# Kernel tuning notes

Hardware: AMD Instinct MI355X
Metric: run time of the kernel (lower is better)

The kernel has to match this reference:

```python
import jax, jax.numpy as jnp
import numpy as np
from jax import lax

B, Ltok, DIM = 8, 4096, 384
D_STATE, D_CONV, EXPAND = 64, 4, 2
D_IN = EXPAND * DIM              # 768
DT_RANK = (DIM + 15) // 16       # 24
HID = 4 * DIM                    # 1536


def setup_inputs() -> dict:
    key = jax.random.key(0)
    ks = jax.random.split(key, 16)
    std = 0.02
    inp = {
        "x": jax.random.normal(ks[0], (B, Ltok, DIM), jnp.float32),
        "h": 64,
        "w": 64,
        # MambaLayer: pre-norm
        "gamma1": jnp.ones((DIM,), jnp.float32),
        "beta1": jnp.zeros((DIM,), jnp.float32),
        # Mamba params
        "W_in": jax.random.normal(ks[1], (2 * D_IN, DIM), jnp.float32) * std,
        "conv_w": jax.random.normal(ks[2], (D_IN, D_CONV), jnp.float32) * (1.0 / np.sqrt(D_CONV)),
        "conv_b": jnp.zeros((D_IN,), jnp.float32),
        "W_xproj": jax.random.normal(ks[3], (DT_RANK + 2 * D_STATE, D_IN), jnp.float32) * std,
        "W_dt": jax.random.normal(ks[4], (D_IN, DT_RANK), jnp.float32) * (DT_RANK ** -0.5),
        "b_dt": jax.random.uniform(ks[5], (D_IN,), jnp.float32, -4.0, -2.0),  # softplus -> small dt
        "A_log": jnp.tile(jnp.log(jnp.arange(1, D_STATE + 1, dtype=jnp.float32)), (D_IN, 1)),
        "Dp": jnp.ones((D_IN,), jnp.float32),
        "W_out": jax.random.normal(ks[6], (DIM, D_IN), jnp.float32) * std,
        # FFN branch
        "gamma2": jnp.ones((DIM,), jnp.float32),
        "beta2": jnp.zeros((DIM,), jnp.float32),
        "W1": jax.random.normal(ks[7], (HID, DIM), jnp.float32) * std,
        "b1": jnp.zeros((HID,), jnp.float32),
        "dw_w": jax.random.normal(ks[8], (HID, 3, 3), jnp.float32) * np.sqrt(2.0 / 9.0),
        "dw_b": jnp.zeros((HID,), jnp.float32),
        "W2": jax.random.normal(ks[9], (DIM, HID), jnp.float32) * std,
        "b2": jnp.zeros((DIM,), jnp.float32),
    }
    return inp


def _layer_norm(x, g, b, eps=1e-5):
    mu = x.mean(-1, keepdims=True)
    var = ((x - mu) ** 2).mean(-1, keepdims=True)
    return (x - mu) * lax.rsqrt(var + eps) * g + b


def _mamba(xn, W_in, conv_w, conv_b, W_xproj, W_dt, b_dt, A_log, Dp, W_out):
    b = xn.shape[0]
    xz = xn @ W_in.T                      # (b, l, 2*d_in)
    xr, z = jnp.split(xz, 2, axis=-1)
    # causal depthwise conv over seq
    xc = jnp.transpose(xr, (0, 2, 1))     # (b, d_in, l)
    xc = lax.conv_general_dilated(xc, conv_w[:, None, :], (1,), [(D_CONV - 1, 0)],
                                  feature_group_count=D_IN) + conv_b[None, :, None]
    xc = jax.nn.silu(jnp.transpose(xc, (0, 2, 1)))  # (b, l, d_in)
    xdb = xc @ W_xproj.T                  # (b, l, dt_rank + 2*d_state)
    dt = jax.nn.softplus(xdb[..., :DT_RANK] @ W_dt.T + b_dt)          # (b, l, d_in)
    Bm = xdb[..., DT_RANK:DT_RANK + D_STATE]                          # (b, l, d_state)
    Cm = xdb[..., DT_RANK + D_STATE:]                                 # (b, l, d_state)
    A = -jnp.exp(A_log)                   # (d_in, d_state)

    def step(hst, inp):
        dt_t, B_t, C_t, x_t = inp         # (b,d_in),(b,ds),(b,ds),(b,d_in)
        dA = jnp.exp(dt_t[..., None] * A)                 # (b, d_in, d_state)
        hst = hst * dA + (dt_t * x_t)[..., None] * B_t[:, None, :]
        y = jnp.einsum('bds,bs->bd', hst, C_t)
        return hst, y

    h0 = jnp.zeros((b, D_IN, D_STATE), xn.dtype)
    seq = (jnp.moveaxis(dt, 1, 0), jnp.moveaxis(Bm, 1, 0),
           jnp.moveaxis(Cm, 1, 0), jnp.moveaxis(xc, 1, 0))
    _, ys = lax.scan(step, h0, seq)
    y = jnp.moveaxis(ys, 0, 1) + xc * Dp  # (b, l, d_in)
    y = y * jax.nn.silu(z)
    return y @ W_out.T


def reference(x, h, w, gamma1, beta1, W_in, conv_w, conv_b, W_xproj, W_dt, b_dt,
              A_log, Dp, W_out, gamma2, beta2, W1, b1, dw_w, dw_b, W2, b2):
    b, n, c = x.shape
    # Mamba branch (MambaLayer: LN then Mamba)
    x = x + _mamba(_layer_norm(x, gamma1, beta1), W_in, conv_w, conv_b,
                   W_xproj, W_dt, b_dt, A_log, Dp, W_out)
    # FFN branch (norm2 -> fc1 -> dwconv -> gelu -> fc2)
    xn = _layer_norm(x, gamma2, beta2)
    f = xn @ W1.T + b1                    # (b, n, HID)
    fm = jnp.transpose(f, (0, 2, 1)).reshape(b, HID, h, w)
    fm = lax.conv_general_dilated(fm, dw_w[:, None, :, :], (1, 1), [(1, 1), (1, 1)],
                                  feature_group_count=HID) + dw_b[None, :, None, None]
    f = jnp.transpose(fm.reshape(b, HID, n), (0, 2, 1))
    f = jax.nn.gelu(f, approximate=False)  # torch nn.GELU default = exact erf
    f = f @ W2.T + b2
    return x + f
```

## Files before the change

kernel.cpp:

```cpp
#include <hip/hip_runtime.h>
#include <math.h>


using u16 = unsigned short;
typedef __bf16 bf8_t __attribute__((ext_vector_type(8)));
typedef float f32x4 __attribute__((ext_vector_type(4)));
typedef float f32x2 __attribute__((ext_vector_type(2)));

#define NT    32768
#define LSEQ  4096
#define DIMC  384
#define DIN   768
#define HIDC  1536
#define NCH   32
#define LCH   128
#define TSTEP 8
#define NTILE (LCH / TSTEP)
#define L2E   1.4426950408889634f

__device__ __forceinline__ float bf2f(u16 u) {
  return __uint_as_float(((unsigned int)u) << 16);
}
__device__ __forceinline__ u16 f2b(float f) {
  unsigned int x = __float_as_uint(f);
  return (u16)((x + 0x7FFFu + ((x >> 16) & 1u)) >> 16);
}
__device__ __forceinline__ float lo16f(unsigned int u) {
  return __uint_as_float(u << 16);
}
__device__ __forceinline__ float hi16f(unsigned int u) {
  return __uint_as_float(u & 0xFFFF0000u);
}

#if __has_builtin(__builtin_elementwise_fma)
#define PKFMA(a, b, c) __builtin_elementwise_fma((a), (b), (c))
#else
__device__ __forceinline__ f32x2 pkfma_(f32x2 a, f32x2 b, f32x2 c) {
  f32x2 d;
  asm("v_pk_fma_f32 %0, %1, %2, %3" : "=v"(d) : "v"(a), "v"(b), "v"(c));
  return d;
}
#define PKFMA(a, b, c) pkfma_((a), (b), (c))
#endif

#define GLDS16(gp, lp)                                                      \
  __builtin_amdgcn_global_load_lds(                                         \
      (const __attribute__((address_space(1))) unsigned int*)(gp),          \
      (__attribute__((address_space(3))) unsigned int*)(lp), 16, 0, 0)

#define OFF_R0   0ull
#define OFF_XC   50331648ull
#define OFF_XDB  100663296ull
#define OFF_DTA  110624768ull
#define OFF_XN   112721920ull
#define OFF_Y    137887744ull
#define OFF_X2   188219392ull
#define OFF_WB   238551040ull
#define OFF_HEND  OFF_X2
#define OFF_WSSUM (OFF_X2 + 25165824ull)
#define OFF_XDBF  (OFF_X2 + 26214400ull)
#define OFF_CWT   OFF_X2
#define OFF_WWT   154664960ull
#define WOF_WIN  0
#define WOF_WXP  589824
#define WOF_WOUT 706560
#define WOF_W1   1001472
#define WOF_W2   1591296
#define WOF_WDT  2181120
#define W_TOTAL  2205696

__global__ __launch_bounds__(256)
void convert_w_k(const float* __restrict__ Win, const float* __restrict__ Wxp,
                 const float* __restrict__ Wout, const float* __restrict__ W1,
                 const float* __restrict__ W2, const float* __restrict__ Wdt,
                 u16* __restrict__ dst) {
  int i = blockIdx.x * 256 + threadIdx.x;
  float v;
  if (i < WOF_WXP)       v = Win[i];
  else if (i < WOF_WOUT) v = Wxp[i - WOF_WXP];
  else if (i < WOF_W1)   v = Wout[i - WOF_WOUT];
  else if (i < WOF_W2)   v = W1[i - WOF_W1];
  else if (i < WOF_WDT) {
    int j = i - WOF_W2;
    int h = j / 294912; int rem = j - h * 294912;
    int r = rem / 768;  int k = rem - r * 768;
    v = W2[r * 1536 + h * 768 + k];
  } else {
    int j = i - WOF_WDT; int c = j & 31; int r = j >> 5;
    v = (c < 24) ? Wdt[r * 24 + c] : 0.f;
  }
  dst[i] = f2b(v);
}

__global__ __launch_bounds__(256)
void tw_k(const float* __restrict__ src, float* __restrict__ dst,
          int rows, int cols) {
  const int i = blockIdx.x * 256 + threadIdx.x;
  if (i < rows * cols) {
    const int r = i / cols, c = i - r * cols;
    dst[(size_t)c * rows + r] = src[i];
  }
}

__global__ __launch_bounds__(256)
void ln_k(const float* __restrict__ x, const float* __restrict__ g,
          const float* __restrict__ b, u16* __restrict__ out) {
  const int row  = (blockIdx.x << 2) + (threadIdx.x >> 6);
  const int lane = threadIdx.x & 63;
  const float* xr = x + (size_t)row * DIMC;
  float v[6]; float s = 0.f;
#pragma unroll
  for (int j = 0; j < 6; ++j) { v[j] = xr[lane + (j << 6)]; s += v[j]; }
#pragma unroll
  for (int m = 1; m < 64; m <<= 1) s += __shfl_xor(s, m);
  const float mu = s * (1.f / DIMC);
  float q = 0.f;
#pragma unroll
  for (int j = 0; j < 6; ++j) { float dv = v[j] - mu; q += dv * dv; }
#pragma unroll
  for (int m = 1; m < 64; m <<= 1) q += __shfl_xor(q, m);
  const float rs = rsqrtf(q * (1.f / DIMC) + 1e-5f);
  u16* orow = out + (size_t)row * DIMC;
#pragma unroll
  for (int j = 0; j < 6; ++j) {
    int c = lane + (j << 6);
    orow[c] = f2b((v[j] - mu) * rs * g[c] + b[c]);
  }
}

template<int OUT_BF16, int ACT>
__global__ __launch_bounds__(256)
void gemm128_k(const u16* __restrict__ A, const u16* __restrict__ Bw,
               void* __restrict__ Cout, const float* __restrict__ bias,
               const float* __restrict__ resid, int N, int K,
               u16* __restrict__ out2, const u16* __restrict__ xc_in) {
  __shared__ __align__(16) u16 As[4096];
  __shared__ __align__(16) u16 Bs[4096];
  const int tid  = threadIdx.x;
  const int lane = tid & 63;
  const int wave = tid >> 6;
  const int bm = blockIdx.y << 7;
  const int bn = blockIdx.x << 7;
  const int wm = (wave >> 1) << 6;
  const int wn = (wave & 1) << 6;
  const int fr = lane & 15;
  const int fq = lane >> 4;
  const int ch0 = tid;
  const int ch1 = tid + 256;
  const int r0c = ch0 >> 2, c0c = (ch0 & 3) << 3;
  const int r1c = ch1 >> 2, c1c = (ch1 & 3) << 3;
  f32x4 acc[4][4] = {};
  for (int k0 = 0; k0 < K; k0 += 32) {
    GLDS16(A + (size_t)(bm + r0c) * K + k0 + c0c, As + ch0 * 8);
    GLDS16(A + (size_t)(bm + r1c) * K + k0 + c1c, As + ch1 * 8);
    GLDS16(Bw + (size_t)(bn + r0c) * K + k0 + c0c, Bs + ch0 * 8);
    GLDS16(Bw + (size_t)(bn + r1c) * K + k0 + c1c, Bs + ch1 * 8);
    __syncthreads();
    bf8_t a[4], b[4];
#pragma unroll
    for (int i = 0; i < 4; ++i)
      a[i] = *(const bf8_t*)&As[(wm + (i << 4) + fr) * 32 + (fq << 3)];
#pragma unroll
    for (int j = 0; j < 4; ++j)
      b[j] = *(const bf8_t*)&Bs[(wn + (j << 4) + fr) * 32 + (fq << 3)];
#pragma unroll
    for (int i = 0; i < 4; ++i)
#pragma unroll
      for (int j = 0; j < 4; ++j)
        acc[i][j] = __builtin_amdgcn_mfma_f32_16x16x32_bf16(a[i], b[j], acc[i][j], 0, 0, 0);
    __syncthreads();
  }
#pragma unroll
  for (int i = 0; i < 4; ++i) {
#pragma unroll
    for (int j = 0; j < 4; ++j) {
      const int col = bn + wn + (j << 4) + fr;
      if (col >= N) continue;
      const float bv = (ACT == 3) ? 0.f : (bias ? bias[col] : 0.f);
#pragma unroll
      for (int r = 0; r < 4; ++r) {
        const int row = bm + wm + (i << 4) + (fq << 2) + r;
        const size_t off = (size_t)row * N + col;
        float v = acc[i][j][r] + bv;
        if (ACT == 2) {
          const float sp = (v > 20.f) ? v : log1pf(__expf(v));
          ((u16*)Cout)[off] = f2b(sp * L2E);
          out2[off] = f2b(sp * bf2f(xc_in[off]));
        } else if (ACT == 3) {
          const float sig = v / (1.f + __expf(-v));
          const float Dv = bias[col];
          out2[off] = f2b((bf2f(out2[off]) + bf2f(xc_in[off]) * Dv) * sig);
        } else if (ACT == 4) {
          ((float*)Cout)[off] = v;
          if (col < 24) out2[(size_t)row * 32 + col] = f2b(v);
        } else {
          if (resid) v += resid[off];
          if (ACT == 1) v = (v > 20.f) ? v : log1pf(__expf(v));
          if (OUT_BF16) ((u16*)Cout)[off] = f2b(v);
          else          ((float*)Cout)[off] = v;
        }
      }
    }
  }
}

__global__ __launch_bounds__(256)
void conv_silu_k(const u16* __restrict__ xr, const float* __restrict__ cwT,
                 const float* __restrict__ cb, u16* __restrict__ xc) {
  const unsigned idx = blockIdx.x * 256 + threadIdx.x;
  const int g = idx % 96;
  const unsigned row = idx / 96;
  const int d0 = g << 3;
  const int t = row & (LSEQ - 1);
  float acc[8];
  {
    const float4 b0 = *(const float4*)(cb + d0);
    const float4 b1 = *(const float4*)(cb + d0 + 4);
    acc[0] = b0.x; acc[1] = b0.y; acc[2] = b0.z; acc[3] = b0.w;
    acc[4] = b1.x; acc[5] = b1.y; acc[6] = b1.z; acc[7] = b1.w;
  }
#pragma unroll
  for (int j = 0; j < 4; ++j) {
    const int tt = t - 3 + j;
    if (tt < 0) continue;
    const uint4 xv = *(const uint4*)(xr + ((size_t)row - 3 + j) * DIN + d0);
    const float4 w0 = *(const float4*)(cwT + j * DIN + d0);
    const float4 w1 = *(const float4*)(cwT + j * DIN + d0 + 4);
    acc[0] = fmaf(lo16f(xv.x), w0.x, acc[0]);
    acc[1] = fmaf(hi16f(xv.x), w0.y, acc[1]);
    acc[2] = fmaf(lo16f(xv.y), w0.z, acc[2]);
    acc[3] = fmaf(hi16f(xv.y), w0.w, acc[3]);
    acc[4] = fmaf(lo16f(xv.z), w1.x, acc[4]);
    acc[5] = fmaf(hi16f(xv.z), w1.y, acc[5]);
    acc[6] = fmaf(lo16f(xv.w), w1.z, acc[6]);
    acc[7] = fmaf(hi16f(xv.w), w1.w, acc[7]);
  }
#define SIL(k) (acc[k] / (1.f + __expf(-acc[k])))
  const ushort4 o0 = make_ushort4(f2b(SIL(0)), f2b(SIL(1)), f2b(SIL(2)), f2b(SIL(3)));
  const ushort4 o1 = make_ushort4(f2b(SIL(4)), f2b(SIL(5)), f2b(SIL(6)), f2b(SIL(7)));
#undef SIL
  u16* po = xc + (size_t)row * DIN + d0;
  *(ushort4*)po = o0;
  *(ushort4*)(po + 4) = o1;
}

__global__ __launch_bounds__(256, 4)
void scan_p1_k(const u16* __restrict__ wA, const u16* __restrict__ dtx,
               const float* __restrict__ xdbF, const float* __restrict__ A_log,
               u16* __restrict__ hend, float* __restrict__ wssum) {
  __shared__ __align__(16) float sB[2][TSTEP][64];
  __shared__ __align__(16) u16  swa[2][TSTEP][256];
  __shared__ __align__(16) u16  sdx[2][TSTEP][256];
  const int id   = blockIdx.x;
  const int dblk = id >> 8;
  const int ccb  = id & 255;
  const int cc   = ccb >> 3;
  const int b    = ccb & 7;
  const int dbase = dblk << 8;
  const int tid  = threadIdx.x;
  const int lane = tid & 63;
  const int wave = tid >> 6;
  const int sg = lane & 3, dg = lane >> 2;
  const int ld0 = (wave << 6) + (dg << 2);
  const int d0  = dbase + ld0;
  const int s16 = sg << 4;
  const size_t row0 = (size_t)b * LSEQ + (size_t)cc * LCH;
  float A1[4];
#pragma unroll
  for (int k = 0; k < 4; ++k) A1[k] = -__expf(A_log[((d0 + k) << 6) + s16]);
  const u16* gW = wA  + (row0 + (tid >> 5)) * DIN + dbase + ((tid & 31) << 3);
  const u16* gX = dtx + (row0 + (tid >> 5)) * DIN + dbase + ((tid & 31) << 3);
  char* lW = (char*)&swa[0][0][0] + tid * 16;
  char* lX = (char*)&sdx[0][0][0] + tid * 16;
  const float* gB = xdbF + (row0 + (tid >> 4)) * 152 + 24 + ((tid & 15) << 2);
  char* lB = (char*)&sB[0][0][0] + tid * 16;
#define P1_STAGE(tile, buf)                                                  \
  GLDS16(gW + (size_t)(tile) * TSTEP * DIN, lW + (buf) * 4096);              \
  GLDS16(gX + (size_t)(tile) * TSTEP * DIN, lX + (buf) * 4096);              \
  if (tid < 128) GLDS16(gB + (size_t)(tile) * TSTEP * 152, lB + (buf) * 2048);
  f32x2 h[4][8] = {};
  float ds[4] = {0.f, 0.f, 0.f, 0.f};
  P1_STAGE(0, 0);
  __syncthreads();
  for (int tile = 0; tile < NTILE; ++tile) {
    const int buf = tile & 1;
    if (tile + 1 < NTILE) { P1_STAGE(tile + 1, buf ^ 1); }
#pragma unroll 4
    for (int t = 0; t < TSTEP; ++t) {
      const ushort4 wv  = *(const ushort4*)&swa[buf][t][ld0];
      const ushort4 xvv = *(const ushort4*)&sdx[buf][t][ld0];
      f32x2 Bv[8];
      *(float4*)&Bv[0] = *(const float4*)&sB[buf][t][s16];
      *(float4*)&Bv[2] = *(const float4*)&sB[buf][t][s16 + 4];
      *(float4*)&Bv[4] = *(const float4*)&sB[buf][t][s16 + 8];
      *(float4*)&Bv[6] = *(const float4*)&sB[buf][t][s16 + 12];
#pragma unroll
      for (int k = 0; k < 4; ++k) {
        const float aw = bf2f(((const u16*)&wv)[k]);
        const float xv = bf2f(((const u16*)&xvv)[k]);
        const float e   = __builtin_amdgcn_exp2f(-aw);
        const float dA0 = __builtin_amdgcn_exp2f(aw * A1[k]);
        const float es  = e * e;
        f32x2 dA2; dA2[0] = dA0; dA2[1] = dA0 * e;
        f32x2 e22; e22[0] = es;  e22[1] = es;
        f32x2 xv2; xv2[0] = xv;  xv2[1] = xv;
        f32x2 (&hh)[8] = h[k];
#pragma unroll
        for (int j = 0; j < 8; ++j) {
          hh[j] = PKFMA(hh[j], dA2, xv2 * Bv[j]);
          if (j < 7) dA2 = dA2 * e22;
        }
        ds[k] += aw;
      }
    }
    __syncthreads();
  }
#pragma unroll
  for (int k = 0; k < 4; ++k) {
    const size_t hb = ((size_t)((cc << 3) + b) * DIN + (d0 + k)) * 64 + s16;
    *(ushort4*)(hend + hb)      = make_ushort4(f2b(h[k][0][0]), f2b(h[k][0][1]), f2b(h[k][1][0]), f2b(h[k][1][1]));
    *(ushort4*)(hend + hb + 4)  = make_ushort4(f2b(h[k][2][0]), f2b(h[k][2][1]), f2b(h[k][3][0]), f2b(h[k][3][1]));
    *(ushort4*)(hend + hb + 8)  = make_ushort4(f2b(h[k][4][0]), f2b(h[k][4][1]), f2b(h[k][5][0]), f2b(h[k][5][1]));
    *(ushort4*)(hend + hb + 12) = make_ushort4(f2b(h[k][6][0]), f2b(h[k][6][1]), f2b(h[k][7][0]), f2b(h[k][7][1]));
  }
  if (sg == 0)
    *(float4*)&wssum[(size_t)((cc << 3) + b) * DIN + d0] =
        make_float4(ds[0], ds[1], ds[2], ds[3]);
}

__global__ __launch_bounds__(256)
void scan_comb_k(const float* __restrict__ A_log,
                 const float* __restrict__ wssum, u16* __restrict__ hend) {
  const int idx = blockIdx.x * 256 + threadIdx.x;
  const int s  = idx & 63;
  const int bd = idx >> 6;
  const int d  = bd % DIN;
  const float A = -__expf(A_log[(d << 6) + s]);
  float h = 0.f;
#pragma unroll
  for (int c = 0; c < NCH; ++c) {
    u16* p = hend + (size_t)c * 393216 + idx;
    const float e = bf2f(*p);
    *p = f2b(h);
    h = h * __builtin_amdgcn_exp2f(A * wssum[c * 6144 + bd]) + e;
  }
}

__global__ __launch_bounds__(256, 4)
void scan_p2_k(const u16* __restrict__ wA, const u16* __restrict__ dtx,
               const float* __restrict__ xdbF, const float* __restrict__ A_log,
               const u16* __restrict__ hin, u16* __restrict__ y) {
  __shared__ __align__(16) float sB[2][TSTEP][64];
  __shared__ __align__(16) float sC[2][TSTEP][64];
  __shared__ __align__(16) u16  swa[2][TSTEP][256];
  __shared__ __align__(16) u16  sdx[2][TSTEP][256];
  const int id   = blockIdx.x;
  const int dblk = id >> 8;
  const int ccb  = id & 255;
  const int cc   = ccb >> 3;
  const int b    = ccb & 7;
  const int dbase = dblk << 8;
  const int tid  = threadIdx.x;
  const int lane = tid & 63;
  const int wave = tid >> 6;
  const int sg = lane & 3, dg = lane >> 2;
  const int ld0 = (wave << 6) + (dg << 2);
  const int d0  = dbase + ld0;
  const int s16 = sg << 4;
  const size_t row0 = (size_t)b * LSEQ + (size_t)cc * LCH;
  float A1[4];
#pragma unroll
  for (int k = 0; k < 4; ++k) A1[k] = -__expf(A_log[((d0 + k) << 6) + s16]);
  f32x2 h[4][8];
#pragma unroll
  for (int k = 0; k < 4; ++k) {
    const size_t hb = ((size_t)((cc << 3) + b) * DIN + (d0 + k)) * 64 + s16;
    const uint4 q0 = *(const uint4*)(hin + hb);
    const uint4 q1 = *(const uint4*)(hin + hb + 8);
    h[k][0][0] = lo16f(q0.x); h[k][0][1] = hi16f(q0.x);
    h[k][1][0] = lo16f(q0.y); h[k][1][1] = hi16f(q0.y);
    h[k][2][0] = lo16f(q0.z); h[k][2][1] = hi16f(q0.z);
    h[k][3][0] = lo16f(q0.w); h[k][3][1] = hi16f(q0.w);
    h[k][4][0] = lo16f(q1.x); h[k][4][1] = hi16f(q1.x);
    h[k][5][0] = lo16f(q1.y); h[k][5][1] = hi16f(q1.y);
    h[k][6][0] = lo16f(q1.z); h[k][6][1] = hi16f(q1.z);
    h[k][7][0] = lo16f(q1.w); h[k][7][1] = hi16f(q1.w);
  }
  const u16* gW = wA  + (row0 + (tid >> 5)) * DIN + dbase + ((tid & 31) << 3);
  const u16* gX = dtx + (row0 + (tid >> 5)) * DIN + dbase + ((tid & 31) << 3);
  char* lW = (char*)&swa[0][0][0] + tid * 16;
  char* lX = (char*)&sdx[0][0][0] + tid * 16;
  const int q7 = tid & 127;
  const float* gQ = xdbF + (row0 + (q7 >> 4)) * 152 + 24 +
                    ((tid < 128) ? 0 : 64) + ((q7 & 15) << 2);
  char* lQ = (char*)((tid < 128) ? &sB[0][0][0] : &sC[0][0][0]) + q7 * 16;
#define P2_STAGE(tile, buf)                                                  \
  GLDS16(gW + (size_t)(tile) * TSTEP * DIN, lW + (buf) * 4096);              \
  GLDS16(gX + (size_t)(tile) * TSTEP * DIN, lX + (buf) * 4096);              \
  GLDS16(gQ + (size_t)(tile) * TSTEP * 152, lQ + (buf) * 2048);
  u16* py = y + row0 * DIN + d0;
  P2_STAGE(0, 0);
  __syncthreads();
  for (int tile = 0; tile < NTILE; ++tile) {
    const int buf = tile & 1;
    if (tile + 1 < NTILE) { P2_STAGE(tile + 1, buf ^ 1); }
#pragma unroll 2
    for (int t = 0; t < TSTEP; ++t) {
      const ushort4 wv  = *(const ushort4*)&swa[buf][t][ld0];
      const ushort4 xvv = *(const ushort4*)&sdx[buf][t][ld0];
      f32x2 Bv[8], Cv[8];
      *(float4*)&Bv[0] = *(const float4*)&sB[buf][t][s16];
      *(float4*)&Bv[2] = *(const float4*)&sB[buf][t][s16 + 4];
      *(float4*)&Bv[4] = *(const float4*)&sB[buf][t][s16 + 8];
      *(float4*)&Bv[6] = *(const float4*)&sB[buf][t][s16 + 12];
      *(float4*)&Cv[0] = *(const float4*)&sC[buf][t][s16];
      *(float4*)&Cv[2] = *(const float4*)&sC[buf][t][s16 + 4];
      *(float4*)&Cv[4] = *(const float4*)&sC[buf][t][s16 + 8];
      *(float4*)&Cv[6] = *(const float4*)&sC[buf][t][s16 + 12];
      float pout[4];
#pragma unroll
      for (int k = 0; k < 4; ++k) {
        const float aw = bf2f(((const u16*)&wv)[k]);
        const float xv = bf2f(((const u16*)&xvv)[k]);
        const float e   = __builtin_amdgcn_exp2f(-aw);
        const float dA0 = __builtin_amdgcn_exp2f(aw * A1[k]);
        const float es  = e * e;
        f32x2 dA2; dA2[0] = dA0; dA2[1] = dA0 * e;
        f32x2 e22; e22[0] = es;  e22[1] = es;
        f32x2 xv2; xv2[0] = xv;  xv2[1] = xv;
        f32x2 (&hh)[8] = h[k];
        f32x2 pa, pb;
#pragma unroll
        for (int j = 0; j < 8; ++j) {
          hh[j] = PKFMA(hh[j], dA2, xv2 * Bv[j]);
          if (j == 0)            pa = hh[0] * Cv[0];
          else if (j == 1)       pb = hh[1] * Cv[1];
          else if ((j & 1) == 0) pa = PKFMA(hh[j], Cv[j], pa);
          else                   pb = PKFMA(hh[j], Cv[j], pb);
          if (j < 7) dA2 = dA2 * e22;
        }
        const f32x2 ps = pa + pb;
        pout[k] = ps[0] + ps[1];
      }
#pragma unroll
      for (int k = 0; k < 4; ++k) {
        pout[k] += __shfl_xor(pout[k], 1);
        pout[k] += __shfl_xor(pout[k], 2);
      }
      if (sg == 0)
        *(ushort4*)py = make_ushort4(f2b(pout[0]), f2b(pout[1]),
                                     f2b(pout[2]), f2b(pout[3]));
      py += DIN;
    }
    __syncthreads();
  }
}

__global__ __launch_bounds__(256)
void dw_gelu_k(const u16* __restrict__ f1, const float* __restrict__ wwT,
               const float* __restrict__ wb, u16* __restrict__ f2h, int co) {
  const unsigned idx = blockIdx.x * 256 + threadIdx.x;
  const int g = idx % 96;
  const unsigned row = idx / 96;
  const int c0 = co + (g << 3);
  const int n = row & (LSEQ - 1);
  const unsigned bb = row >> 12;
  const int i = n >> 6, jj = n & 63;
  float acc[8];
  {
    const float4 b0 = *(const float4*)(wb + c0);
    const float4 b1 = *(const float4*)(wb + c0 + 4);
    acc[0] = b0.x; acc[1] = b0.y; acc[2] = b0.z; acc[3] = b0.w;
    acc[4] = b1.x; acc[5] = b1.y; acc[6] = b1.z; acc[7] = b1.w;
  }
#pragma unroll
  for (int di = -1; di <= 1; ++di) {
    const int ii = i + di;
    if (ii < 0 || ii > 63) continue;
#pragma unroll
    for (int dj = -1; dj <= 1; ++dj) {
      const int j2 = jj + dj;
      if (j2 < 0 || j2 > 63) continue;
      const size_t r2 = ((size_t)bb << 12) + ((size_t)ii << 6) + j2;
      const uint4 xv = *(const uint4*)(f1 + r2 * HIDC + c0);
      const int tt = (di + 1) * 3 + (dj + 1);
      const float4 w0 = *(const float4*)(wwT + tt * HIDC + c0);
      const float4 w1 = *(const float4*)(wwT + tt * HIDC + c0 + 4);
      acc[0] = fmaf(lo16f(xv.x), w0.x, acc[0]);
      acc[1] = fmaf(hi16f(xv.x), w0.y, acc[1]);
      acc[2] = fmaf(lo16f(xv.y), w0.z, acc[2]);
      acc[3] = fmaf(hi16f(xv.y), w0.w, acc[3]);
      acc[4] = fmaf(lo16f(xv.z), w1.x, acc[4]);
      acc[5] = fmaf(hi16f(xv.z), w1.y, acc[5]);
      acc[6] = fmaf(lo16f(xv.w), w1.z, acc[6]);
      acc[7] = fmaf(hi16f(xv.w), w1.w, acc[7]);
    }
  }
#define GEL(k) (0.5f * acc[k] * (1.f + erff(acc[k] * 0.70710678118654752f)))
  const ushort4 o0 = make_ushort4(f2b(GEL(0)), f2b(GEL(1)), f2b(GEL(2)), f2b(GEL(3)));
  const ushort4 o1 = make_ushort4(f2b(GEL(4)), f2b(GEL(5)), f2b(GEL(6)), f2b(GEL(7)));
#undef GEL
  u16* po = f2h + (size_t)row * DIN + (g << 3);
  *(ushort4*)po = o0;
  *(ushort4*)(po + 4) = o1;
}

extern "C" void kernel_launch(void* const* d_in, const int* in_sizes, int n_in,
                              void* d_out, int out_size, void* d_ws, size_t ws_size,
                              hipStream_t stream) {
  const float* x     = (const float*)d_in[0];
  const float* g1    = (const float*)d_in[3];
  const float* be1   = (const float*)d_in[4];
  const float* W_in  = (const float*)d_in[5];
  const float* convw = (const float*)d_in[6];
  const float* convb = (const float*)d_in[7];
  const float* W_xp  = (const float*)d_in[8];
  const float* W_dt  = (const float*)d_in[9];
  const float* b_dt  = (const float*)d_in[10];
  const float* A_log = (const float*)d_in[11];
  const float* Dp    = (const float*)d_in[12];
  const float* W_out = (const float*)d_in[13];
  const float* g2    = (const float*)d_in[14];
  const float* be2   = (const float*)d_in[15];
  const float* W1    = (const float*)d_in[16];
  const float* b1    = (const float*)d_in[17];
  const float* dww   = (const float*)d_in[18];
  const float* dwb   = (const float*)d_in[19];
  const float* W2    = (const float*)d_in[20];
  const float* b2    = (const float*)d_in[21];
  float* out = (float*)d_out;

  char* ws = (char*)d_ws;
  u16*   r0    = (u16*)(ws + OFF_R0);
  u16*   xc_b  = (u16*)(ws + OFF_XC);
  u16*   dtA_b = (u16*)(ws + OFF_DTA);
  u16*   xn_b  = (u16*)(ws + OFF_XN);
  u16*   y_b   = (u16*)(ws + OFF_Y);
  float* x2    = (float*)(ws + OFF_X2);
  u16*   hendb = (u16*)(ws + OFF_HEND);
  float* wssum = (float*)(ws + OFF_WSSUM);
  float* xdbF  = (float*)(ws + OFF_XDBF);
  float* cwT   = (float*)(ws + OFF_CWT);
  float* wwT   = (float*)(ws + OFF_WWT);
  u16*   wb    = (u16*)(ws + OFF_WB);
  u16*   f1_b  = r0;
  u16*   f2h_b = (u16*)(ws + OFF_XDB);

  convert_w_k<<<W_TOTAL / 256, 256, 0, stream>>>(W_in, W_xp, W_out, W1, W2, W_dt, wb);
  tw_k<<<12, 256, 0, stream>>>(convw, cwT, DIN, 4);
  ln_k<<<NT / 4, 256, 0, stream>>>(x, g1, be1, xn_b);
  gemm128_k<1, 0><<<dim3(6, 256), 256, 0, stream>>>(xn_b, wb + WOF_WIN, r0, nullptr, nullptr, DIN, DIMC, nullptr, nullptr);
  conv_silu_k<<<(NT * 96) / 256, 256, 0, stream>>>(r0, cwT, convb, xc_b);
  gemm128_k<0, 4><<<dim3(2, 256), 256, 0, stream>>>(xc_b, wb + WOF_WXP, xdbF, nullptr, nullptr, 152, DIN, dtA_b, nullptr);
  gemm128_k<1, 2><<<dim3(6, 256), 256, 0, stream>>>(dtA_b, wb + WOF_WDT, r0, b_dt, nullptr, DIN, 32, y_b, xc_b);
  scan_p1_k<<<768, 256, 0, stream>>>(r0, y_b, xdbF, A_log, hendb, wssum);
  scan_comb_k<<<393216 / 256, 256, 0, stream>>>(A_log, wssum, hendb);
  scan_p2_k<<<768, 256, 0, stream>>>(r0, y_b, xdbF, A_log, hendb, y_b);
  gemm128_k<1, 3><<<dim3(6, 256), 256, 0, stream>>>(xn_b, wb + WOF_WIN + 294912, y_b, Dp, nullptr, DIN, DIMC, y_b, xc_b);
  gemm128_k<0, 0><<<dim3(3, 256), 256, 0, stream>>>(y_b, wb + WOF_WOUT, x2, nullptr, x, DIMC, DIN, nullptr, nullptr);
  tw_k<<<54, 256, 0, stream>>>(dww, wwT, HIDC, 9);
  ln_k<<<NT / 4, 256, 0, stream>>>(x2, g2, be2, xn_b);
  gemm128_k<1, 0><<<dim3(12, 256), 256, 0, stream>>>(xn_b, wb + WOF_W1, f1_b, b1, nullptr, HIDC, DIMC, nullptr, nullptr);
  dw_gelu_k<<<(NT * 96) / 256, 256, 0, stream>>>(f1_b, wwT, dwb, f2h_b, 0);
  gemm128_k<0, 0><<<dim3(3, 256), 256, 0, stream>>>(f2h_b, wb + WOF_W2, out, b2, x2, DIMC, DIN, nullptr, nullptr);
  dw_gelu_k<<<(NT * 96) / 256, 256, 0, stream>>>(f1_b, wwT, dwb, f2h_b, DIN);
  gemm128_k<0, 0><<<dim3(3, 256), 256, 0, stream>>>(f2h_b, wb + WOF_W2 + 294912, out, nullptr, out, DIMC, DIN, nullptr, nullptr);
}
```

Baseline: 1.140 ms.

## Replace LDS tile staging in scan kernels with direct register double-buffered global loads

Both chunked selective-scan passes drop their shared-memory double buffers and the async global-to-LDS staging with per-tile barriers. Each thread now loads its own B/C, dt-weight and x values straight from global memory into registers, one timestep ahead, with a two-slot software pipeline. The launch-bounds occupancy hint drops from 4 to 3 blocks to make room for the extra registers. This removes LDS traffic and __syncthreads stalls, but relies on the caches for B/C vectors that are now redundantly loaded by many threads, and each load has only one timestep of latency hiding.

```diff
diff --git a/kernel.cpp b/kernel.cpp
--- a/kernel.cpp
+++ b/kernel.cpp
@@ -14,8 +14,6 @@
 #define HIDC  1536
 #define NCH   32
 #define LCH   128
-#define TSTEP 8
-#define NTILE (LCH / TSTEP)
 #define L2E   1.4426950408889634f
 
 __device__ __forceinline__ float bf2f(u16 u) {
@@ -244,13 +242,10 @@
   *(ushort4*)(po + 4) = o1;
 }
 
-__global__ __launch_bounds__(256, 4)
+__global__ __launch_bounds__(256, 3)
 void scan_p1_k(const u16* __restrict__ wA, const u16* __restrict__ dtx,
                const float* __restrict__ xdbF, const float* __restrict__ A_log,
                u16* __restrict__ hend, float* __restrict__ wssum) {
-  __shared__ __align__(16) float sB[2][TSTEP][64];
-  __shared__ __align__(16) u16  swa[2][TSTEP][256];
-  __shared__ __align__(16) u16  sdx[2][TSTEP][256];
   const int id   = blockIdx.x;
   const int dblk = id >> 8;
   const int ccb  = id & 255;
@@ -268,52 +263,54 @@
   float A1[4];
 #pragma unroll
   for (int k = 0; k < 4; ++k) A1[k] = -__expf(A_log[((d0 + k) << 6) + s16]);
-  const u16* gW = wA  + (row0 + (tid >> 5)) * DIN + dbase + ((tid & 31) << 3);
-  const u16* gX = dtx + (row0 + (tid >> 5)) * DIN + dbase + ((tid & 31) << 3);
-  char* lW = (char*)&swa[0][0][0] + tid * 16;
-  char* lX = (char*)&sdx[0][0][0] + tid * 16;
-  const float* gB = xdbF + (row0 + (tid >> 4)) * 152 + 24 + ((tid & 15) << 2);
-  char* lB = (char*)&sB[0][0][0] + tid * 16;
-#define P1_STAGE(tile, buf)                                                  \
-  GLDS16(gW + (size_t)(tile) * TSTEP * DIN, lW + (buf) * 4096);              \
-  GLDS16(gX + (size_t)(tile) * TSTEP * DIN, lX + (buf) * 4096);              \
-  if (tid < 128) GLDS16(gB + (size_t)(tile) * TSTEP * 152, lB + (buf) * 2048);
+  const float* pB = xdbF + row0 * 152 + 24 + s16;
+  const u16*  pW = wA  + row0 * DIN + d0;
+  const u16*  pX = dtx + row0 * DIN + d0;
+  float4 Bq[2][4]; ushort4 wq[2], xq[2];
   f32x2 h[4][8] = {};
   float ds[4] = {0.f, 0.f, 0.f, 0.f};
-  P1_STAGE(0, 0);
-  __syncthreads();
-  for (int tile = 0; tile < NTILE; ++tile) {
-    const int buf = tile & 1;
-    if (tile + 1 < NTILE) { P1_STAGE(tile + 1, buf ^ 1); }
-#pragma unroll 4
-    for (int t = 0; t < TSTEP; ++t) {
-      const ushort4 wv  = *(const ushort4*)&swa[buf][t][ld0];
-      const ushort4 xvv = *(const ushort4*)&sdx[buf][t][ld0];
-      f32x2 Bv[8];
-      *(float4*)&Bv[0] = *(const float4*)&sB[buf][t][s16];
-      *(float4*)&Bv[2] = *(const float4*)&sB[buf][t][s16 + 4];
-      *(float4*)&Bv[4] = *(const float4*)&sB[buf][t][s16 + 8];
-      *(float4*)&Bv[6] = *(const float4*)&sB[buf][t][s16 + 12];
-#pragma unroll
-      for (int k = 0; k < 4; ++k) {
-        const float aw = bf2f(((const u16*)&wv)[k]);
-        const float xv = bf2f(((const u16*)&xvv)[k]);
-        const float e   = __builtin_amdgcn_exp2f(-aw);
-        const float dA0 = __builtin_amdgcn_exp2f(aw * A1[k]);
-        const float es  = e * e;
-        f32x2 dA2; dA2[0] = dA0; dA2[1] = dA0 * e;
-        f32x2 e22; e22[0] = es;  e22[1] = es;
-        f32x2 xv2; xv2[0] = xv;  xv2[1] = xv;
-        f32x2 (&hh)[8] = h[k];
-#pragma unroll
-        for (int j = 0; j < 8; ++j) {
-          hh[j] = PKFMA(hh[j], dA2, xv2 * Bv[j]);
-          if (j < 7) dA2 = dA2 * e22;
-        }
-        ds[k] += aw;
-      }
-    }
-    __syncthreads();
+#define P1_LOAD(sl, t)                                                      \
+  { const float* bp = pB + (size_t)(t) * 152;                               \
+    Bq[sl][0] = *(const float4*)(bp);                                       \
+    Bq[sl][1] = *(const float4*)(bp + 4);                                   \
+    Bq[sl][2] = *(const float4*)(bp + 8);                                   \
+    Bq[sl][3] = *(const float4*)(bp + 12);                                  \
+    wq[sl] = *(const ushort4*)(pW + (size_t)(t) * DIN);                     \
+    xq[sl] = *(const ushort4*)(pX + (size_t)(t) * DIN); }
+#define P1_BODY(sl)                                                         \
+  { const ushort4 wv = wq[sl];                                              \
+    const ushort4 xvv = xq[sl];                                             \
+    f32x2 Bv[8];                                                            \
+    _Pragma("unroll")                                                       \
+    for (int i = 0; i < 4; ++i) {                                           \
+      Bv[2*i][0] = Bq[sl][i].x;   Bv[2*i][1] = Bq[sl][i].y;                 \
+      Bv[2*i+1][0] = Bq[sl][i].z; Bv[2*i+1][1] = Bq[sl][i].w;               \
+    }                                                                       \
+    _Pragma("unroll")                                                       \
+    for (int k = 0; k < 4; ++k) {                                           \
+      const float aw = bf2f(((const u16*)&wv)[k]);                          \
+      const float xv = bf2f(((const u16*)&xvv)[k]);                         \
+      const float e   = __builtin_amdgcn_exp2f(-aw);                        \
+      const float dA0 = __builtin_amdgcn_exp2f(aw * A1[k]);                 \
+      const float es  = e * e;                                              \
+      f32x2 dA2; dA2[0] = dA0; dA2[1] = dA0 * e;                            \
+      f32x2 e22; e22[0] = es;  e22[1] = es;                                 \
+      f32x2 xv2; xv2[0] = xv;  xv2[1] = xv;                                 \
+      f32x2 (&hh)[8] = h[k];                                                \
+      _Pragma("unroll")                                                     \
+      for (int j = 0; j < 8; ++j) {                                         \
+        hh[j] = PKFMA(hh[j], dA2, xv2 * Bv[j]);                             \
+        if (j < 7) dA2 = dA2 * e22;                                         \
+      }                                                                     \
+      ds[k] += aw;                                                          \
+    } }
+  P1_LOAD(0, 0);
+  for (int t2 = 0; t2 < LCH / 2; ++t2) {
+    const int t = t2 << 1;
+    P1_LOAD(1, t + 1);
+    P1_BODY(0);
+    if (t2 + 1 < LCH / 2) { P1_LOAD(0, t + 2); }
+    P1_BODY(1);
   }
 #pragma unroll
   for (int k = 0; k < 4; ++k) {
@@ -346,14 +343,10 @@
   }
 }
 
-__global__ __launch_bounds__(256, 4)
+__global__ __launch_bounds__(256, 3)
 void scan_p2_k(const u16* __restrict__ wA, const u16* __restrict__ dtx,
                const float* __restrict__ xdbF, const float* __restrict__ A_log,
                const u16* __restrict__ hin, u16* __restrict__ y) {
-  __shared__ __align__(16) float sB[2][TSTEP][64];
-  __shared__ __align__(16) float sC[2][TSTEP][64];
-  __shared__ __align__(16) u16  swa[2][TSTEP][256];
-  __shared__ __align__(16) u16  sdx[2][TSTEP][256];
   const int id   = blockIdx.x;
   const int dblk = id >> 8;
   const int ccb  = id & 255;
@@ -386,73 +379,75 @@
     h[k][6][0] = lo16f(q1.z); h[k][6][1] = hi16f(q1.z);
     h[k][7][0] = lo16f(q1.w); h[k][7][1] = hi16f(q1.w);
   }
-  const u16* gW = wA  + (row0 + (tid >> 5)) * DIN + dbase + ((tid & 31) << 3);
-  const u16* gX = dtx + (row0 + (tid >> 5)) * DIN + dbase + ((tid & 31) << 3);
-  char* lW = (char*)&swa[0][0][0] + tid * 16;
-  char* lX = (char*)&sdx[0][0][0] + tid * 16;
-  const int q7 = tid & 127;
-  const float* gQ = xdbF + (row0 + (q7 >> 4)) * 152 + 24 +
-                    ((tid < 128) ? 0 : 64) + ((q7 & 15) << 2);
-  char* lQ = (char*)((tid < 128) ? &sB[0][0][0] : &sC[0][0][0]) + q7 * 16;
-#define P2_STAGE(tile, buf)                                                  \
-  GLDS16(gW + (size_t)(tile) * TSTEP * DIN, lW + (buf) * 4096);              \
-  GLDS16(gX + (size_t)(tile) * TSTEP * DIN, lX + (buf) * 4096);              \
-  GLDS16(gQ + (size_t)(tile) * TSTEP * 152, lQ + (buf) * 2048);
+  const float* pB = xdbF + row0 * 152 + 24 + s16;
+  const u16*  pW = wA  + row0 * DIN + d0;
+  const u16*  pX = dtx + row0 * DIN + d0;
   u16* py = y + row0 * DIN + d0;
-  P2_STAGE(0, 0);
-  __syncthreads();
-  for (int tile = 0; tile < NTILE; ++tile) {
-    const int buf = tile & 1;
-    if (tile + 1 < NTILE) { P2_STAGE(tile + 1, buf ^ 1); }
-#pragma unroll 2
-    for (int t = 0; t < TSTEP; ++t) {
-      const ushort4 wv  = *(const ushort4*)&swa[buf][t][ld0];
-      const ushort4 xvv = *(const ushort4*)&sdx[buf][t][ld0];
-      f32x2 Bv[8], Cv[8];
-      *(float4*)&Bv[0] = *(const float4*)&sB[buf][t][s16];
-      *(float4*)&Bv[2] = *(const float4*)&sB[buf][t][s16 + 4];
-      *(float4*)&Bv[4] = *(const float4*)&sB[buf][t][s16 + 8];
-      *(float4*)&Bv[6] = *(const float4*)&sB[buf][t][s16 + 12];
-      *(float4*)&Cv[0] = *(const float4*)&sC[buf][t][s16];
-      *(float4*)&Cv[2] = *(const float4*)&sC[buf][t][s16 + 4];
-      *(float4*)&Cv[4] = *(const float4*)&sC[buf][t][s16 + 8];
-      *(float4*)&Cv[6] = *(const float4*)&sC[buf][t][s16 + 12];
-      float pout[4];
-#pragma unroll
-      for (int k = 0; k < 4; ++k) {
-        const float aw = bf2f(((const u16*)&wv)[k]);
-        const float xv = bf2f(((const u16*)&xvv)[k]);
-        const float e   = __builtin_amdgcn_exp2f(-aw);
-        const float dA0 = __builtin_amdgcn_exp2f(aw * A1[k]);
-        const float es  = e * e;
-        f32x2 dA2; dA2[0] = dA0; dA2[1] = dA0 * e;
-        f32x2 e22; e22[0] = es;  e22[1] = es;
-        f32x2 xv2; xv2[0] = xv;  xv2[1] = xv;
-        f32x2 (&hh)[8] = h[k];
-        f32x2 pa, pb;
-#pragma unroll
-        for (int j = 0; j < 8; ++j) {
-          hh[j] = PKFMA(hh[j], dA2, xv2 * Bv[j]);
-          if (j == 0)            pa = hh[0] * Cv[0];
-          else if (j == 1)       pb = hh[1] * Cv[1];
-          else if ((j & 1) == 0) pa = PKFMA(hh[j], Cv[j], pa);
-          else                   pb = PKFMA(hh[j], Cv[j], pb);
-          if (j < 7) dA2 = dA2 * e22;
-        }
-        const f32x2 ps = pa + pb;
-        pout[k] = ps[0] + ps[1];
-      }
-#pragma unroll
-      for (int k = 0; k < 4; ++k) {
-        pout[k] += __shfl_xor(pout[k], 1);
-        pout[k] += __shfl_xor(pout[k], 2);
-      }
-      if (sg == 0)
-        *(ushort4*)py = make_ushort4(f2b(pout[0]), f2b(pout[1]),
-                                     f2b(pout[2]), f2b(pout[3]));
-      py += DIN;
-    }
-    __syncthreads();
+  float4 Bq[2][4], Cq[2][4]; ushort4 wq[2], xq[2];
+#define P2_LOAD(sl, t)                                                      \
+  { const float* bp = pB + (size_t)(t) * 152;                               \
+    Bq[sl][0] = *(const float4*)(bp);                                       \
+    Bq[sl][1] = *(const float4*)(bp + 4);                                   \
+    Bq[sl][2] = *(const float4*)(bp + 8);                                   \
+    Bq[sl][3] = *(const float4*)(bp + 12);                                  \
+    Cq[sl][0] = *(const float4*)(bp + 64);                                  \
+    Cq[sl][1] = *(const float4*)(bp + 68);                                  \
+    Cq[sl][2] = *(const float4*)(bp + 72);                                  \
+    Cq[sl][3] = *(const float4*)(bp + 76);                                  \
+    wq[sl] = *(const ushort4*)(pW + (size_t)(t) * DIN);                     \
+    xq[sl] = *(const ushort4*)(pX + (size_t)(t) * DIN); }
+#define P2_BODY(sl)                                                         \
+  { const ushort4 wv = wq[sl];                                              \
+    const ushort4 xvv = xq[sl];                                             \
+    f32x2 Bv[8], Cv[8];                                                     \
+    _Pragma("unroll")                                                       \
+    for (int i = 0; i < 4; ++i) {                                           \
+      Bv[2*i][0] = Bq[sl][i].x;   Bv[2*i][1] = Bq[sl][i].y;                 \
+      Bv[2*i+1][0] = Bq[sl][i].z; Bv[2*i+1][1] = Bq[sl][i].w;               \
+      Cv[2*i][0] = Cq[sl][i].x;   Cv[2*i][1] = Cq[sl][i].y;                 \
+      Cv[2*i+1][0] = Cq[sl][i].z; Cv[2*i+1][1] = Cq[sl][i].w;               \
+    }                                                                       \
+    float pout[4];                                                          \
+    _Pragma("unroll")                                                       \
+    for (int k = 0; k < 4; ++k) {                                           \
+      const float aw = bf2f(((const u16*)&wv)[k]);                          \
+      const float xv = bf2f(((const u16*)&xvv)[k]);                         \
+      const float e   = __builtin_amdgcn_exp2f(-aw);                        \
+      const float dA0 = __builtin_amdgcn_exp2f(aw * A1[k]);                 \
+      const float es  = e * e;                                              \
+      f32x2 dA2; dA2[0] = dA0; dA2[1] = dA0 * e;                            \
+      f32x2 e22; e22[0] = es;  e22[1] = es;                                 \
+      f32x2 xv2; xv2[0] = xv;  xv2[1] = xv;                                 \
+      f32x2 (&hh)[8] = h[k];                                                \
+      f32x2 pa, pb;                                                         \
+      _Pragma("unroll")                                                     \
+      for (int j = 0; j < 8; ++j) {                                         \
+        hh[j] = PKFMA(hh[j], dA2, xv2 * Bv[j]);                             \
+        if (j == 0)            pa = hh[0] * Cv[0];                          \
+        else if (j == 1)       pb = hh[1] * Cv[1];                          \
+        else if ((j & 1) == 0) pa = PKFMA(hh[j], Cv[j], pa);                \
+        else                   pb = PKFMA(hh[j], Cv[j], pb);                \
+        if (j < 7) dA2 = dA2 * e22;                                         \
+      }                                                                     \
+      const f32x2 ps = pa + pb;                                             \
+      pout[k] = ps[0] + ps[1];                                              \
+    }                                                                       \
+    _Pragma("unroll")                                                       \
+    for (int k = 0; k < 4; ++k) {                                           \
+      pout[k] += __shfl_xor(pout[k], 1);                                    \
+      pout[k] += __shfl_xor(pout[k], 2);                                    \
+    }                                                                       \
+    if (sg == 0)                                                            \
+      *(ushort4*)py = make_ushort4(f2b(pout[0]), f2b(pout[1]),              \
+                                   f2b(pout[2]), f2b(pout[3]));             \
+    py += DIN; }
+  P2_LOAD(0, 0);
+  for (int t2 = 0; t2 < LCH / 2; ++t2) {
+    const int t = t2 << 1;
+    P2_LOAD(1, t + 1);
+    P2_BODY(0);
+    if (t2 + 1 < LCH / 2) { P2_LOAD(0, t + 2); }
+    P2_BODY(1);
   }
 }
 
```

Result: slower. 1.170 ms (+2.7%).
